# Performance work log

Hardware: AMD Instinct MI355X
Metric: run time of the kernel (lower is better)

The kernel has to match this reference:

```python
import jax, jax.numpy as jnp
import numpy as np

L, D, H, F_IN = 3, 256, 8, 5
HD = D // H
FF = 4 * D
EPS = 1e-5


def _layer_norm(x, g, b):
    mu = jnp.mean(x, axis=-1, keepdims=True)
    var = jnp.mean(jnp.square(x - mu), axis=-1, keepdims=True)
    return (x - mu) * jax.lax.rsqrt(var + EPS) * g + b


def setup_inputs() -> dict:
    key = jax.random.key(0)
    ks = jax.random.split(key, 20)
    s = 0.02
    inp = {
        'x': jax.random.normal(ks[0], (32, 512, F_IN), jnp.float32),
        'mask': jax.random.randint(ks[1], (32, 512), 0, 2) == 1,
        'Win': jax.random.normal(ks[2], (F_IN, D), jnp.float32) * s,
        'bin_': jnp.zeros((D,), jnp.float32),
        'Wq': jax.random.normal(ks[3], (L, D, D), jnp.float32) * s,
        'bq': jnp.zeros((L, D), jnp.float32),
        'Wk': jax.random.normal(ks[4], (L, D, D), jnp.float32) * s,
        'bk': jnp.zeros((L, D), jnp.float32),
        'Wv': jax.random.normal(ks[5], (L, D, D), jnp.float32) * s,
        'bv': jnp.zeros((L, D), jnp.float32),
        'Wo': jax.random.normal(ks[6], (L, D, D), jnp.float32) * s,
        'bo': jnp.zeros((L, D), jnp.float32),
        'g1': jnp.ones((L, D), jnp.float32),
        'b1': jnp.zeros((L, D), jnp.float32),
        'W1': jax.random.normal(ks[7], (L, D, FF), jnp.float32) * s,
        'c1': jnp.zeros((L, FF), jnp.float32),
        'W2': jax.random.normal(ks[8], (L, FF, D), jnp.float32) * s,
        'c2': jnp.zeros((L, D), jnp.float32),
        'g2': jnp.ones((L, D), jnp.float32),
        'b2': jnp.zeros((L, D), jnp.float32),
    }
    return inp


def reference(x, mask, Win, bin_, Wq, bq, Wk, bk, Wv, bv, Wo, bo, g1, b1, W1, c1, W2, c2, g2, b2):
    B, S, _ = x.shape
    scale = 1.0 / jnp.sqrt(jnp.float32(HD))
    h = x @ Win + bin_  # [B,S,D]
    kmask = mask[:, None, None, :]  # [B,1,1,S] key-padding mask
    for l in range(L):
        q = (h @ Wq[l] + bq[l]).reshape(B, S, H, HD).transpose(0, 2, 1, 3)
        k = (h @ Wk[l] + bk[l]).reshape(B, S, H, HD).transpose(0, 2, 1, 3)
        v = (h @ Wv[l] + bv[l]).reshape(B, S, H, HD).transpose(0, 2, 1, 3)
        scores = jnp.einsum('bhqd,bhkd->bhqk', q, k) * scale
        scores = jnp.where(kmask, -jnp.inf, scores)
        attn = jnp.nan_to_num(jax.nn.softmax(scores, axis=-1), nan=0.0)
        ao = jnp.einsum('bhqk,bhkd->bhqd', attn, v).transpose(0, 2, 1, 3).reshape(B, S, D)
        ao = ao @ Wo[l] + bo[l]
        h = _layer_norm(h + ao, g1[l], b1[l])
        ff = jax.nn.relu(h @ W1[l] + c1[l]) @ W2[l] + c2[l]
        h = _layer_norm(h + ff, g2[l], b2[l])
    return h
```

## Files before the change

kernel.cpp:

```cpp
#include <hip/hip_runtime.h>
#include <cstdint>

#define NLAYER 3
#define DMODEL 256
#define NHEAD 8
#define HEADD 32
#define FFDIM 1024
#define BATCH 32
#define SEQ 512
#define MTOK (BATCH*SEQ)

typedef __attribute__((ext_vector_type(8))) __bf16 bf16x8;
typedef __attribute__((ext_vector_type(4))) __bf16 bf16x4;
typedef __attribute__((ext_vector_type(4))) float f32x4;
typedef __attribute__((ext_vector_type(16))) float f32x16;

typedef __attribute__((address_space(1))) const uint8_t ga_t;
typedef __attribute__((address_space(3))) uint8_t la_t;
__device__ __forceinline__ void gll16(const void* g, void* l) {
    __builtin_amdgcn_global_load_lds((ga_t*)g, (la_t*)l, 16, 0, 0);
}

__global__ __launch_bounds__(256)
void prep_kernel(const float* __restrict__ Wq, const float* __restrict__ Wk,
                 const float* __restrict__ Wv, const float* __restrict__ Wo,
                 const float* __restrict__ W1, const float* __restrict__ W2,
                 const float* __restrict__ bq, const float* __restrict__ bk,
                 const float* __restrict__ bv,
                 __bf16* __restrict__ wqf, __bf16* __restrict__ wot,
                 __bf16* __restrict__ w1f, __bf16* __restrict__ w2f,
                 float* __restrict__ bqkv,
                 const float* __restrict__ x, const float* __restrict__ Win,
                 const float* __restrict__ bin, __bf16* __restrict__ h16)
{
    const int bid = blockIdx.x;
    const int tid = threadIdx.x;
    if (bid >= 2313) {
        const int m0 = (bid - 2313) * 8;
        const float bv_ = bin[tid];
#pragma unroll
        for (int p = 0; p < 8; ++p) {
            const int m = m0 + p;
            const float* xr = x + (size_t)m * 5;
            float acc = bv_;
#pragma unroll
            for (int k = 0; k < 5; ++k) acc += xr[k] * Win[k * DMODEL + tid];
            h16[(size_t)m * DMODEL + tid] = (__bf16)acc;
        }
        return;
    }
    if (bid >= 3 * 768) {
        int idx = (bid - 3 * 768) * 256 + tid;
        int l = idx / 768, j = idx % 768;
        float v = (j < 256) ? bq[l * 256 + j]
                : (j < 512) ? bk[l * 256 + j - 256]
                            : bv[l * 256 + j - 512];
        bqkv[idx] = v;
        return;
    }
    const int l = bid / 768;
    const int rr = bid % 768;
    __shared__ float tile[32][33];
    const int c = tid & 31, rbase = tid >> 5;

    if (rr < 192) {
        const int ty = rr >> 6;
        const int t = rr & 63;
        const float* src = (ty == 0 ? Wq : ty == 1 ? Wk : Wv) + (size_t)l * 65536;
        const int tk = t >> 3, tj = t & 7;
#pragma unroll
        for (int p = 0; p < 4; ++p) {
            int kr = rbase + p * 8;
            tile[kr][c] = src[(size_t)(tk * 32 + kr) * 256 + tj * 32 + c];
        }
        __syncthreads();
        if (tid < 128) {
            const int lane = tid & 63, ksl = tid >> 6;
            const int cl = lane & 31, kh = lane >> 5;
            bf16x8 v;
#pragma unroll
            for (int j = 0; j < 8; ++j) v[j] = (__bf16)tile[ksl * 16 + kh * 8 + j][cl];
            *(bf16x8*)(wqf + ((size_t)(((l * 8 + tj) * 3 + ty) * 16
                              + tk * 2 + ksl)) * 512 + lane * 8) = v;
        }
        return;
    }
    if (rr < 256) {
        const int t = rr - 192;
        const float* src = Wo + (size_t)l * 65536;
        __bf16* dst = wot + (size_t)l * 65536;
        const int tk = t >> 3, tj = t & 7;
#pragma unroll
        for (int p = 0; p < 4; ++p) {
            int kr = rbase + p * 8;
            tile[kr][c] = src[(size_t)(tk * 32 + kr) * 256 + tj * 32 + c];
        }
        __syncthreads();
#pragma unroll
        for (int p = 0; p < 4; ++p) {
            int nr = rbase + p * 8;
            dst[(size_t)(tj * 32 + nr) * 256 + tk * 32 + c] = (__bf16)tile[c][nr];
        }
        return;
    }
    const float* src; int NN, tk, tj, t;
    if (rr < 512) { t = rr - 256; src = W1 + (size_t)l * 262144;
                    NN = 1024; tk = t >> 5; tj = t & 31; }
    else          { t = rr - 512; src = W2 + (size_t)l * 262144;
                    NN = 256;  tk = t >> 3; tj = t & 7; }
#pragma unroll
    for (int p = 0; p < 4; ++p) {
        int kr = rbase + p * 8;
        tile[kr][c] = src[(size_t)(tk * 32 + kr) * NN + tj * 32 + c];
    }
    __syncthreads();
    if (tid < 128) {
        const int sub = tid >> 6, lane = tid & 63;
        const int fq = lane >> 4, ff = lane & 15;
        bf16x8 v;
#pragma unroll
        for (int j = 0; j < 8; ++j) v[j] = (__bf16)tile[fq * 8 + j][sub * 16 + ff];
        if (rr < 512)
            *(bf16x8*)(w1f + ((size_t)(l * 64 + tj * 2 + sub) * 8 + tk) * 512 + lane * 8) = v;
        else
            *(bf16x8*)(w2f + ((size_t)(l * 16 + tj * 2 + sub) * 32 + tk) * 512 + lane * 8) = v;
    }
}

__global__ __launch_bounds__(1024)
void attn_kernel(const __bf16* __restrict__ hA, const __bf16* __restrict__ wqf,
                 const float* __restrict__ bqkv, const int* __restrict__ mask,
                 __bf16* __restrict__ ao)
{
    __shared__ __bf16 Ks[512 * 40];
    __shared__ __bf16 Vt[32 * 520];
    __shared__ __attribute__((aligned(16))) __bf16 Un[3*16*512];
    __shared__ float maskadd[512];

    const int b = blockIdx.x >> 3;
    const int h = blockIdx.x & 7;
    const int t = threadIdx.x;
    const int lane = t & 63;
    const int wave = t >> 6;
    const int cl = lane & 31;
    const int kh = lane >> 5;
    const float scale = 0.17677669529663687f;

    {
        const __bf16* wsrc = wqf + (size_t)h * 24576;
#pragma unroll
        for (int p = 0; p < 3; ++p) {
            const int chunk = p * 1024 + t;
            gll16(wsrc + (size_t)chunk * 8, Un + (p * 1024 + wave * 64) * 8);
        }
    }
    if (t < 512) maskadd[t] = mask[b * SEQ + t] ? -1e30f : 0.f;
    __syncthreads();

    const int tok0 = wave * 32;
    const size_t arow = ((size_t)(b * SEQ + tok0 + cl)) * 256;
    f32x16 aQ, aK, aV;
#pragma unroll
    for (int i = 0; i < 16; ++i) { aQ[i] = 0.f; aK[i] = 0.f; aV[i] = 0.f; }
#pragma unroll
    for (int ks = 0; ks < 16; ++ks) {
        bf16x8 tf = *(const bf16x8*)(hA + arow + ks * 16 + kh * 8);
        bf16x8 wq = *(const bf16x8*)(Un + (0 * 16 + ks) * 512 + lane * 8);
        bf16x8 wk = *(const bf16x8*)(Un + (1 * 16 + ks) * 512 + lane * 8);
        bf16x8 wv = *(const bf16x8*)(Un + (2 * 16 + ks) * 512 + lane * 8);
        aQ = __builtin_amdgcn_mfma_f32_32x32x16_bf16(wq, tf, aQ, 0, 0, 0);
        aK = __builtin_amdgcn_mfma_f32_32x32x16_bf16(wk, tf, aK, 0, 0, 0);
        aV = __builtin_amdgcn_mfma_f32_32x32x16_bf16(wv, tf, aV, 0, 0, 0);
    }
#pragma unroll
    for (int r = 0; r < 16; ++r) {
        const int rdim = (r & 3) + 8 * (r >> 2) + 4 * kh;
        Ks[(tok0 + cl) * 40 + rdim] = (__bf16)(aK[r] + bqkv[256 + h * 32 + rdim]);
        Vt[rdim * 520 + tok0 + cl]  = (__bf16)(aV[r] + bqkv[512 + h * 32 + rdim]);
    }
    __syncthreads();

    __bf16* Pw = Un + wave * 1024;
#pragma unroll
    for (int r = 0; r < 16; ++r) {
        const int rdim = (r & 3) + 8 * (r >> 2) + 4 * kh;
        Pw[cl * 32 + rdim] = (__bf16)(aQ[r] + bqkv[h * 32 + rdim]);
    }
    bf16x8 qf0 = *(const bf16x8*)(Pw + cl * 32 + kh * 8);
    bf16x8 qf1 = *(const bf16x8*)(Pw + cl * 32 + 16 + kh * 8);
    __syncthreads();

    f32x16 oacc;
#pragma unroll
    for (int i = 0; i < 16; ++i) oacc[i] = 0.f;
    float lsum = 0.f;

    for (int kt = 0; kt < SEQ; kt += 32) {
        bf16x8 kf0 = *(const bf16x8*)(Ks + (kt + cl) * 40 + kh * 8);
        bf16x8 kf1 = *(const bf16x8*)(Ks + (kt + cl) * 40 + 16 + kh * 8);
        f32x16 s;
#pragma unroll
        for (int i = 0; i < 16; ++i) s[i] = 0.f;
        s = __builtin_amdgcn_mfma_f32_32x32x16_bf16(kf0, qf0, s, 0, 0, 0);
        s = __builtin_amdgcn_mfma_f32_32x32x16_bf16(kf1, qf1, s, 0, 0, 0);
        float pv[16];
#pragma unroll
        for (int g = 0; g < 4; ++g) {
            f32x4 mv = *(const f32x4*)(maskadd + kt + 8 * g + 4 * kh);
#pragma unroll
            for (int r = 0; r < 4; ++r) {
                float e = __expf(s[g * 4 + r] * scale + mv[r]);
                pv[g * 4 + r] = e;
                lsum += e;
            }
        }
#pragma unroll
        for (int g = 0; g < 4; ++g) {
            bf16x4 pb;
#pragma unroll
            for (int r = 0; r < 4; ++r) pb[r] = (__bf16)pv[g * 4 + r];
            *(bf16x4*)(Pw + cl * 32 + 8 * g + 4 * kh) = pb;
        }
        bf16x8 pf0 = *(const bf16x8*)(Pw + cl * 32 + kh * 8);
        bf16x8 pf1 = *(const bf16x8*)(Pw + cl * 32 + 16 + kh * 8);
        bf16x8 vf0 = *(const bf16x8*)(Vt + cl * 520 + kt + kh * 8);
        bf16x8 vf1 = *(const bf16x8*)(Vt + cl * 520 + kt + 16 + kh * 8);
        oacc = __builtin_amdgcn_mfma_f32_32x32x16_bf16(vf0, pf0, oacc, 0, 0, 0);
        oacc = __builtin_amdgcn_mfma_f32_32x32x16_bf16(vf1, pf1, oacc, 0, 0, 0);
    }

    lsum += __shfl_xor(lsum, 32);
    const float inv = (lsum > 0.f) ? 1.f / lsum : 0.f;
    __bf16* orow = ao + (size_t)(b * SEQ + tok0 + cl) * DMODEL + h * 32;
#pragma unroll
    for (int g = 0; g < 4; ++g) {
        bf16x4 w;
#pragma unroll
        for (int r = 0; r < 4; ++r) w[r] = (__bf16)(oacc[g * 4 + r] * inv);
        *(bf16x4*)(orow + 8 * g + 4 * kh) = w;
    }
}

template<int LAST>
__global__ __launch_bounds__(256, 4)
void gemm_ln_kernel(const __bf16* __restrict__ A, const __bf16* __restrict__ Bt,
                    const float* __restrict__ bias, const __bf16* __restrict__ res,
                    const float* __restrict__ g, const float* __restrict__ be,
                    __bf16* __restrict__ out16, float* __restrict__ out32, int K)
{
    __shared__ __bf16 As[32 * 64];
    __shared__ __bf16 Bs[256 * 64];
    __shared__ float red[32 * 8];
    const int tid = threadIdx.x;
    const int m0 = blockIdx.x * 32;
    const int lane = tid & 63;
    const int wave = tid >> 6;
    const int wn = wave * 64;
    const int fr = lane & 15;
    const int quad = lane >> 4;
    const int lr = lane >> 3;
    const int qg = (lane & 7) ^ lr;
    const int frs = fr & 7;

    const __bf16* Ab = A  + (size_t)(m0 + wave * 8 + lr) * K + qg * 8;
    const __bf16* Bb = Bt + (size_t)(wave * 64 + lr) * K + qg * 8;

    f32x4 acc[2][4];
#pragma unroll
    for (int i = 0; i < 2; ++i)
#pragma unroll
        for (int j = 0; j < 4; ++j)
#pragma unroll
            for (int r = 0; r < 4; ++r) acc[i][j][r] = 0.f;

    for (int k0 = 0; k0 < K; k0 += 64) {
        gll16(Ab + k0, As + wave * 512);
#pragma unroll
        for (int p = 0; p < 8; ++p)
            gll16(Bb + (size_t)p * 8 * K + k0, Bs + (wave * 8 + p) * 512);
        __syncthreads();
#pragma unroll
        for (int kk = 0; kk < 2; ++kk) {
            bf16x8 af[2], bfr[4];
#pragma unroll
            for (int i = 0; i < 2; ++i) {
                int row = i * 16 + fr;
                af[i] = *(const bf16x8*)(As + row * 64 + (((kk * 4 + quad) ^ frs) * 8));
            }
#pragma unroll
            for (int j = 0; j < 4; ++j) {
                int row = wn + j * 16 + fr;
                bfr[j] = *(const bf16x8*)(Bs + row * 64 + (((kk * 4 + quad) ^ frs) * 8));
            }
#pragma unroll
            for (int i = 0; i < 2; ++i)
#pragma unroll
                for (int j = 0; j < 4; ++j)
                    acc[i][j] = __builtin_amdgcn_mfma_f32_16x16x32_bf16(
                        af[i], bfr[j], acc[i][j], 0, 0, 0);
        }
        __syncthreads();
    }

    float bv[4];
#pragma unroll
    for (int j = 0; j < 4; ++j) bv[j] = bias[wn + j * 16 + fr];

#pragma unroll
    for (int i = 0; i < 2; ++i) {
#pragma unroll
        for (int r = 0; r < 4; ++r) {
            const int row = i * 16 + quad * 4 + r;
            float ps = 0.f, pq = 0.f;
#pragma unroll
            for (int j = 0; j < 4; ++j) {
                const int gc = wn + j * 16 + fr;
                float v = acc[i][j][r] + bv[j]
                        + (float)res[(size_t)(m0 + row) * DMODEL + gc];
                acc[i][j][r] = v;
                ps += v;
                pq += v * v;
            }
#pragma unroll
            for (int off = 1; off < 16; off <<= 1) {
                ps += __shfl_xor(ps, off, 64);
                pq += __shfl_xor(pq, off, 64);
            }
            if (fr == 0) {
                red[row * 8 + wave * 2]     = ps;
                red[row * 8 + wave * 2 + 1] = pq;
            }
        }
    }
    __syncthreads();

#pragma unroll
    for (int i = 0; i < 2; ++i) {
#pragma unroll
        for (int r = 0; r < 4; ++r) {
            const int row = i * 16 + quad * 4 + r;
            f32x4 a = *(const f32x4*)(red + row * 8);
            f32x4 b2 = *(const f32x4*)(red + row * 8 + 4);
            const float s  = a[0] + a[2] + b2[0] + b2[2];
            const float sq = a[1] + a[3] + b2[1] + b2[3];
            const float mu = s * (1.f / DMODEL);
            const float var = sq * (1.f / DMODEL) - mu * mu;
            const float rs = rsqrtf(var + 1e-5f);
#pragma unroll
            for (int j = 0; j < 4; ++j) {
                const int gc = wn + j * 16 + fr;
                float y = (acc[i][j][r] - mu) * rs * g[gc] + be[gc];
                if (LAST) out32[(size_t)(m0 + row) * DMODEL + gc] = y;
                else      out16[(size_t)(m0 + row) * DMODEL + gc] = (__bf16)y;
            }
        }
    }
}

template<int LAST>
__global__ __launch_bounds__(256, 2)
void ff_kernel(const __bf16* __restrict__ A, const __bf16* __restrict__ w1A,
               const float* __restrict__ c1, const __bf16* __restrict__ w2A,
               const float* __restrict__ c2, const __bf16* __restrict__ res,
               const float* __restrict__ g, const float* __restrict__ be,
               __bf16* __restrict__ out16, float* __restrict__ out32)
{
    __shared__ __attribute__((aligned(16))) __bf16 As[4][32 * 64];
    __shared__ __attribute__((aligned(16))) __bf16 P[2][32 * 136];
    __shared__ float c1s[1024];
    __shared__ float red[32 * 8];
    const int tid = threadIdx.x;
    const int lane = tid & 63;
    const int wave = tid >> 6;
    const int fr = lane & 15;
    const int quad = lane >> 4;
    const int m0 = blockIdx.x * 32;

    {
        const int lr = lane >> 3, pos = lane & 7;
#pragma unroll
        for (int c4 = 0; c4 < 4; ++c4) {
            const int row = c4 * 8 + lr;
            const int gsw = pos ^ (row & 7);
            gll16(A + (size_t)(m0 + row) * 256 + wave * 64 + gsw * 8,
                  &As[wave][c4 * 8 * 64]);
        }
    }
    *(f32x4*)(c1s + tid * 4) = *(const f32x4*)(c1 + tid * 4);

    f32x4 acc2[4][2];
#pragma unroll
    for (int jj = 0; jj < 4; ++jj)
#pragma unroll
        for (int tt = 0; tt < 2; ++tt)
#pragma unroll
            for (int r = 0; r < 4; ++r) acc2[jj][tt][r] = 0.f;
    __syncthreads();

#pragma unroll 2
    for (int ch = 0; ch < 8; ++ch) {
        bf16x8 w2r[4][4];
#pragma unroll
        for (int jj = 0; jj < 4; ++jj)
#pragma unroll
            for (int ks = 0; ks < 4; ++ks) {
                const int dt = wave * 4 + jj, kt = ch * 4 + ks;
                w2r[jj][ks] = *(const bf16x8*)(w2A + ((size_t)(dt * 32 + kt) * 64 + lane) * 8);
            }
        f32x4 acc1[2][2];
#pragma unroll
        for (int i = 0; i < 2; ++i)
#pragma unroll
            for (int j = 0; j < 2; ++j)
#pragma unroll
                for (int r = 0; r < 4; ++r) acc1[i][j][r] = 0.f;
#pragma unroll
        for (int ks = 0; ks < 8; ++ks) {
            bf16x8 w1r[2], tf[2];
#pragma unroll
            for (int i = 0; i < 2; ++i) {
                const int ft = ch * 8 + wave * 2 + i;
                w1r[i] = *(const bf16x8*)(w1A + ((size_t)(ft * 8 + ks) * 64 + lane) * 8);
            }
#pragma unroll
            for (int j = 0; j < 2; ++j)
                tf[j] = *(const bf16x8*)(&As[ks >> 1][(j * 16 + fr) * 64
                          + ((((ks & 1) * 4 + quad) ^ (fr & 7)) * 8)]);
#pragma unroll
            for (int i = 0; i < 2; ++i)
#pragma unroll
                for (int j = 0; j < 2; ++j)
                    acc1[i][j] = __builtin_amdgcn_mfma_f32_16x16x32_bf16(
                        w1r[i], tf[j], acc1[i][j], 0, 0, 0);
        }
#pragma unroll
        for (int i = 0; i < 2; ++i) {
            f32x4 cb = *(const f32x4*)(c1s + ch * 128 + wave * 32 + i * 16 + quad * 4);
#pragma unroll
            for (int j = 0; j < 2; ++j) {
                bf16x4 pb;
#pragma unroll
                for (int r = 0; r < 4; ++r)
                    pb[r] = (__bf16)fmaxf(acc1[i][j][r] + cb[r], 0.f);
                *(bf16x4*)(&P[ch & 1][(j * 16 + fr) * 136 + wave * 32 + i * 16 + quad * 4]) = pb;
            }
        }
        __syncthreads();
#pragma unroll
        for (int ks = 0; ks < 4; ++ks) {
            bf16x8 pf[2];
#pragma unroll
            for (int tt = 0; tt < 2; ++tt)
                pf[tt] = *(const bf16x8*)(&P[ch & 1][(tt * 16 + fr) * 136 + ks * 32 + quad * 8]);
#pragma unroll
            for (int jj = 0; jj < 4; ++jj)
#pragma unroll
                for (int tt = 0; tt < 2; ++tt)
                    acc2[jj][tt] = __builtin_amdgcn_mfma_f32_16x16x32_bf16(
                        w2r[jj][ks], pf[tt], acc2[jj][tt], 0, 0, 0);
        }
    }

    float ps0 = 0.f, pq0 = 0.f, ps1 = 0.f, pq1 = 0.f;
#pragma unroll
    for (int jj = 0; jj < 4; ++jj) {
        f32x4 cb = *(const f32x4*)(c2 + wave * 64 + jj * 16 + quad * 4);
#pragma unroll
        for (int tt = 0; tt < 2; ++tt) {
            bf16x4 rv = *(const bf16x4*)(res + (size_t)(m0 + tt * 16 + fr) * DMODEL
                                         + wave * 64 + jj * 16 + quad * 4);
#pragma unroll
            for (int r = 0; r < 4; ++r) {
                float v = acc2[jj][tt][r] + cb[r] + (float)rv[r];
                acc2[jj][tt][r] = v;
                if (tt == 0) { ps0 += v; pq0 += v * v; }
                else         { ps1 += v; pq1 += v * v; }
            }
        }
    }
    ps0 += __shfl_xor(ps0, 16); ps0 += __shfl_xor(ps0, 32);
    pq0 += __shfl_xor(pq0, 16); pq0 += __shfl_xor(pq0, 32);
    ps1 += __shfl_xor(ps1, 16); ps1 += __shfl_xor(ps1, 32);
    pq1 += __shfl_xor(pq1, 16); pq1 += __shfl_xor(pq1, 32);
    if (quad == 0) {
        red[fr * 8 + wave * 2]            = ps0;
        red[fr * 8 + wave * 2 + 1]        = pq0;
        red[(16 + fr) * 8 + wave * 2]     = ps1;
        red[(16 + fr) * 8 + wave * 2 + 1] = pq1;
    }
    __syncthreads();
    float mu[2], rs_[2];
#pragma unroll
    for (int tt = 0; tt < 2; ++tt) {
        const int tok = tt * 16 + fr;
        f32x4 a = *(const f32x4*)(red + tok * 8);
        f32x4 b2 = *(const f32x4*)(red + tok * 8 + 4);
        const float s  = a[0] + a[2] + b2[0] + b2[2];
        const float sq = a[1] + a[3] + b2[1] + b2[3];
        mu[tt] = s * (1.f / DMODEL);
        const float var = sq * (1.f / DMODEL) - mu[tt] * mu[tt];
        rs_[tt] = rsqrtf(var + 1e-5f);
    }
#pragma unroll
    for (int jj = 0; jj < 4; ++jj) {
        f32x4 gv = *(const f32x4*)(g  + wave * 64 + jj * 16 + quad * 4);
        f32x4 bv = *(const f32x4*)(be + wave * 64 + jj * 16 + quad * 4);
#pragma unroll
        for (int tt = 0; tt < 2; ++tt) {
            const size_t base = (size_t)(m0 + tt * 16 + fr) * DMODEL
                              + wave * 64 + jj * 16 + quad * 4;
            if (LAST) {
                f32x4 y;
#pragma unroll
                for (int r = 0; r < 4; ++r)
                    y[r] = (acc2[jj][tt][r] - mu[tt]) * rs_[tt] * gv[r] + bv[r];
                *(f32x4*)(out32 + base) = y;
            } else {
                bf16x4 y;
#pragma unroll
                for (int r = 0; r < 4; ++r)
                    y[r] = (__bf16)((acc2[jj][tt][r] - mu[tt]) * rs_[tt] * gv[r] + bv[r]);
                *(bf16x4*)(out16 + base) = y;
            }
        }
    }
}

extern "C" void kernel_launch(void* const* d_in, const int* in_sizes, int n_in,
                              void* d_out, int out_size, void* d_ws, size_t ws_size,
                              hipStream_t stream)
{
    const float* x   = (const float*)d_in[0];
    const int*   mask= (const int*)d_in[1];
    const float* Win = (const float*)d_in[2];
    const float* bin = (const float*)d_in[3];
    const float* Wq  = (const float*)d_in[4];
    const float* bq  = (const float*)d_in[5];
    const float* Wk  = (const float*)d_in[6];
    const float* bk  = (const float*)d_in[7];
    const float* Wv  = (const float*)d_in[8];
    const float* bv  = (const float*)d_in[9];
    const float* Wo  = (const float*)d_in[10];
    const float* bo  = (const float*)d_in[11];
    const float* g1  = (const float*)d_in[12];
    const float* b1  = (const float*)d_in[13];
    const float* W1  = (const float*)d_in[14];
    const float* c1  = (const float*)d_in[15];
    const float* W2  = (const float*)d_in[16];
    const float* c2  = (const float*)d_in[17];
    const float* g2  = (const float*)d_in[18];
    const float* b2  = (const float*)d_in[19];

    char* ws = (char*)d_ws;
    size_t off = 0;
    auto alloc = [&](size_t bytes) -> void* {
        void* p = ws + off;
        off += (bytes + 255) & ~(size_t)255;
        return p;
    };
    __bf16* hA   = (__bf16*)alloc((size_t)MTOK * 256 * 2);
    __bf16* hB   = (__bf16*)alloc((size_t)MTOK * 256 * 2);
    __bf16* ao   = (__bf16*)alloc((size_t)MTOK * 256 * 2);
    __bf16* wqf  = (__bf16*)alloc((size_t)3 * 8 * 3 * 16 * 512 * 2);
    __bf16* wot  = (__bf16*)alloc((size_t)3 * 256 * 256 * 2);
    __bf16* w1f  = (__bf16*)alloc((size_t)3 * 1024 * 256 * 2);
    __bf16* w2f  = (__bf16*)alloc((size_t)3 * 256 * 1024 * 2);
    float*  bqkv = (float*)alloc((size_t)3 * 768 * 4);

    prep_kernel<<<dim3(2313 + MTOK / 8), dim3(256), 0, stream>>>(
        Wq, Wk, Wv, Wo, W1, W2, bq, bk, bv, wqf, wot, w1f, w2f, bqkv,
        x, Win, bin, hA);

    for (int l = 0; l < NLAYER; ++l) {
        attn_kernel<<<dim3(256), dim3(1024), 0, stream>>>(
            hA, wqf + (size_t)l * 8 * 3 * 16 * 512, bqkv + l * 768, mask, ao);
        gemm_ln_kernel<0><<<dim3(MTOK / 32), dim3(256), 0, stream>>>(
            ao, wot + (size_t)l * 65536, bo + l * 256, hA,
            g1 + l * 256, b1 + l * 256, hB, nullptr, 256);
        if (l == 2) {
            ff_kernel<1><<<dim3(MTOK / 32), dim3(256), 0, stream>>>(
                hB, w1f + (size_t)l * 262144, c1 + l * 1024,
                w2f + (size_t)l * 262144, c2 + l * 256, hB,
                g2 + l * 256, b2 + l * 256, nullptr, (float*)d_out);
        } else {
            ff_kernel<0><<<dim3(MTOK / 32), dim3(256), 0, stream>>>(
                hB, w1f + (size_t)l * 262144, c1 + l * 1024,
                w2f + (size_t)l * 262144, c2 + l * 256, hB,
                g2 + l * 256, b2 + l * 256, hA, nullptr);
        }
    }
}
```

Measured before the change: 345.1 us.

## Compact unmasked keys per batch and skip masked key tiles in attention

A new prep stage computes, for each batch, the compacted position of every unmasked key and the count of unmasked keys, using a wave ballot. The attention kernel scatters K and V only for unmasked tokens into compact slots, zero-pads the tail up to a multiple of 32, and loops only over the populated key tiles. This drops roughly half of the QK and PV work, since the mask is random. The softmax scale is also folded into Q before the loop, and per-batch tile counts now vary, which can unbalance blocks.

```diff
diff --git a/kernel.cpp b/kernel.cpp
--- a/kernel.cpp
+++ b/kernel.cpp
@@ -31,10 +31,29 @@
                  __bf16* __restrict__ w1f, __bf16* __restrict__ w2f,
                  float* __restrict__ bqkv,
                  const float* __restrict__ x, const float* __restrict__ Win,
-                 const float* __restrict__ bin, __bf16* __restrict__ h16)
+                 const float* __restrict__ bin, __bf16* __restrict__ h16,
+                 const int* __restrict__ mask, int* __restrict__ pos,
+                 int* __restrict__ nbp)
 {
     const int bid = blockIdx.x;
     const int tid = threadIdx.x;
+    if (bid >= 4361) {
+        const int b = bid - 4361;
+        if (tid < 64) {
+            int base = 0;
+#pragma unroll
+            for (int c = 0; c < 8; ++c) {
+                const int j = c * 64 + tid;
+                const bool un = (mask[b * SEQ + j] == 0);
+                const unsigned long long bal = __ballot(un);
+                const int p = __popcll(bal & ((1ull << tid) - 1ull));
+                pos[b * SEQ + j] = un ? (base + p) : -1;
+                base += __popcll(bal);
+            }
+            if (tid == 0) nbp[b] = base;
+        }
+        return;
+    }
     if (bid >= 2313) {
         const int m0 = (bid - 2313) * 8;
         const float bv_ = bin[tid];
@@ -129,13 +148,13 @@
 
 __global__ __launch_bounds__(1024)
 void attn_kernel(const __bf16* __restrict__ hA, const __bf16* __restrict__ wqf,
-                 const float* __restrict__ bqkv, const int* __restrict__ mask,
-                 __bf16* __restrict__ ao)
+                 const float* __restrict__ bqkv, const int* __restrict__ pos,
+                 const int* __restrict__ nbp, __bf16* __restrict__ ao)
 {
     __shared__ __bf16 Ks[512 * 40];
     __shared__ __bf16 Vt[32 * 520];
     __shared__ __attribute__((aligned(16))) __bf16 Un[3*16*512];
-    __shared__ float maskadd[512];
+    __shared__ float tailadd[512];
 
     const int b = blockIdx.x >> 3;
     const int h = blockIdx.x & 7;
@@ -146,6 +165,10 @@
     const int kh = lane >> 5;
     const float scale = 0.17677669529663687f;
 
+    const int nb = nbp[b];
+    const int nkt = (nb + 31) & ~31;
+    const int tailN = nkt - nb;
+
     {
         const __bf16* wsrc = wqf + (size_t)h * 24576;
 #pragma unroll
@@ -154,7 +177,17 @@
             gll16(wsrc + (size_t)chunk * 8, Un + (p * 1024 + wave * 64) * 8);
         }
     }
-    if (t < 512) maskadd[t] = mask[b * SEQ + t] ? -1e30f : 0.f;
+    if (t < 512) tailadd[t] = (t < nb) ? 0.f : -1e30f;
+    {
+        if (t < tailN * 64) {
+            const int row = nb + (t >> 6), d = t & 63;
+            if (d < 40) Ks[row * 40 + d] = (__bf16)0.f;
+        }
+        if (t < tailN * 32) {
+            const int col = nb + (t >> 5), d = t & 31;
+            Vt[d * 520 + col] = (__bf16)0.f;
+        }
+    }
     __syncthreads();
 
     const int tok0 = wave * 32;
@@ -172,19 +205,22 @@
         aK = __builtin_amdgcn_mfma_f32_32x32x16_bf16(wk, tf, aK, 0, 0, 0);
         aV = __builtin_amdgcn_mfma_f32_32x32x16_bf16(wv, tf, aV, 0, 0, 0);
     }
+    const int slot = pos[b * SEQ + tok0 + cl];
+    if (slot >= 0) {
+#pragma unroll
+        for (int r = 0; r < 16; ++r) {
+            const int rdim = (r & 3) + 8 * (r >> 2) + 4 * kh;
+            Ks[slot * 40 + rdim] = (__bf16)(aK[r] + bqkv[256 + h * 32 + rdim]);
+            Vt[rdim * 520 + slot] = (__bf16)(aV[r] + bqkv[512 + h * 32 + rdim]);
+        }
+    }
+    __syncthreads();
+
+    __bf16* Pw = Un + wave * 1024;
 #pragma unroll
     for (int r = 0; r < 16; ++r) {
         const int rdim = (r & 3) + 8 * (r >> 2) + 4 * kh;
-        Ks[(tok0 + cl) * 40 + rdim] = (__bf16)(aK[r] + bqkv[256 + h * 32 + rdim]);
-        Vt[rdim * 520 + tok0 + cl]  = (__bf16)(aV[r] + bqkv[512 + h * 32 + rdim]);
-    }
-    __syncthreads();
-
-    __bf16* Pw = Un + wave * 1024;
-#pragma unroll
-    for (int r = 0; r < 16; ++r) {
-        const int rdim = (r & 3) + 8 * (r >> 2) + 4 * kh;
-        Pw[cl * 32 + rdim] = (__bf16)(aQ[r] + bqkv[h * 32 + rdim]);
+        Pw[cl * 32 + rdim] = (__bf16)((aQ[r] + bqkv[h * 32 + rdim]) * scale);
     }
     bf16x8 qf0 = *(const bf16x8*)(Pw + cl * 32 + kh * 8);
     bf16x8 qf1 = *(const bf16x8*)(Pw + cl * 32 + 16 + kh * 8);
@@ -195,7 +231,7 @@
     for (int i = 0; i < 16; ++i) oacc[i] = 0.f;
     float lsum = 0.f;
 
-    for (int kt = 0; kt < SEQ; kt += 32) {
+    for (int kt = 0; kt < nkt; kt += 32) {
         bf16x8 kf0 = *(const bf16x8*)(Ks + (kt + cl) * 40 + kh * 8);
         bf16x8 kf1 = *(const bf16x8*)(Ks + (kt + cl) * 40 + 16 + kh * 8);
         f32x16 s;
@@ -206,10 +242,10 @@
         float pv[16];
 #pragma unroll
         for (int g = 0; g < 4; ++g) {
-            f32x4 mv = *(const f32x4*)(maskadd + kt + 8 * g + 4 * kh);
+            f32x4 mv = *(const f32x4*)(tailadd + kt + 8 * g + 4 * kh);
 #pragma unroll
             for (int r = 0; r < 4; ++r) {
-                float e = __expf(s[g * 4 + r] * scale + mv[r]);
+                float e = __expf(s[g * 4 + r] + mv[r]);
                 pv[g * 4 + r] = e;
                 lsum += e;
             }
@@ -566,14 +602,16 @@
     __bf16* w1f  = (__bf16*)alloc((size_t)3 * 1024 * 256 * 2);
     __bf16* w2f  = (__bf16*)alloc((size_t)3 * 256 * 1024 * 2);
     float*  bqkv = (float*)alloc((size_t)3 * 768 * 4);
-
-    prep_kernel<<<dim3(2313 + MTOK / 8), dim3(256), 0, stream>>>(
+    int*    pos  = (int*)alloc((size_t)BATCH * SEQ * 4);
+    int*    nbp  = (int*)alloc((size_t)BATCH * 4);
+
+    prep_kernel<<<dim3(4393), dim3(256), 0, stream>>>(
         Wq, Wk, Wv, Wo, W1, W2, bq, bk, bv, wqf, wot, w1f, w2f, bqkv,
-        x, Win, bin, hA);
+        x, Win, bin, hA, mask, pos, nbp);
 
     for (int l = 0; l < NLAYER; ++l) {
         attn_kernel<<<dim3(256), dim3(1024), 0, stream>>>(
-            hA, wqf + (size_t)l * 8 * 3 * 16 * 512, bqkv + l * 768, mask, ao);
+            hA, wqf + (size_t)l * 8 * 3 * 16 * 512, bqkv + l * 768, pos, nbp, ao);
         gemm_ln_kernel<0><<<dim3(MTOK / 32), dim3(256), 0, stream>>>(
             ao, wot + (size_t)l * 65536, bo + l * 256, hA,
             g1 + l * 256, b1 + l * 256, hB, nullptr, 256);
```

Measured after the change: 321.8 us. 1.07x faster.
